# Kernel optimization log

Hardware: AMD Instinct MI355X
Metric: run time of the kernel (lower is better)

The kernel has to match this reference:

```python
import jax, jax.numpy as jnp
import numpy as np

VOCAB, F, H1, H2 = 64, 4096, 64, 32   # vocab size, featureVectorSize, hidden dims (hard-coded 64/32/1 in source)
NBBOX, NWORDS = 8192, 16


def _uniform(key, shape, fan_in):
    # torch nn.Linear default init: U(-1/sqrt(fan_in), 1/sqrt(fan_in))
    bound = 1.0 / np.sqrt(fan_in)
    return jax.random.uniform(key, shape, jnp.float32, -bound, bound)


def setup_inputs() -> dict:
    key = jax.random.key(0)
    ks = jax.random.split(key, 8)
    x = jax.random.normal(ks[0], (NBBOX, F), jnp.float32)
    words = jax.random.randint(ks[1], (NWORDS,), 0, VOCAB)  # indices of active word-models
    # Stacked per-word MLP params (one tiny MLP per vocab word)
    W1 = _uniform(ks[2], (VOCAB, F, H1), F)
    b1 = _uniform(ks[3], (VOCAB, H1), F)
    W2 = _uniform(ks[4], (VOCAB, H1, H2), H1)
    b2 = _uniform(ks[5], (VOCAB, H2), H1)
    W3 = _uniform(ks[6], (VOCAB, H2), H2)   # Linear(32,1) weight, squeezed to [VOCAB, H2]
    b3 = _uniform(ks[7], (VOCAB,), H2)
    return {"nBBox": NBBOX, "x": x, "words": words,
            "W1": W1, "b1": b1, "W2": W2, "b2": b2, "W3": W3, "b3": b3}


def reference(nBBox, x, words, W1, b1, W2, b2, W3, b3):
    # Gather the active word-models (dict lookup in the original)
    w1, c1 = W1[words], b1[words]          # [W,F,H1], [W,H1]
    w2, c2 = W2[words], b2[words]          # [W,H1,H2], [W,H2]
    w3, c3 = W3[words], b3[words]          # [W,H2], [W]
    # Batched 3-layer MLP over all active words at once (replaces Python loop)
    h1 = jax.nn.relu(jnp.einsum('bf,wfh->wbh', x, w1) + c1[:, None, :])   # [W,B,H1]
    h2 = jax.nn.relu(jnp.einsum('wbh,whk->wbk', h1, w2) + c2[:, None, :])  # [W,B,H2]
    logits = jnp.einsum('wbk,wk->wb', h2, w3) + c3[:, None]                # [W,B]
    # output = ones(nBBox,1) * prod_w sigmoid(logits_w)
    return jnp.prod(jax.nn.sigmoid(logits), axis=0)[:, None]               # [B,1]
```

## Files before the change

kernel.cpp:

```cpp
#include <hip/hip_runtime.h>
#include <stdint.h>
#include <math.h>

#define NBBOX 8192
#define FDIM  4096
#define H1DIM 64
#define H2DIM 32
#define NW    16

typedef __attribute__((ext_vector_type(8))) _Float16 f16x8;
typedef __attribute__((ext_vector_type(4))) float    f32x4;

typedef __attribute__((address_space(1))) void* gptr_t;
typedef __attribute__((address_space(3))) void* lptr_t;

__device__ __forceinline__ void g2l16(const void* g, void* l) {
    __builtin_amdgcn_global_load_lds((gptr_t)(uintptr_t)g,
                                     (lptr_t)(uint32_t)(uintptr_t)l,
                                     16, 0, 0);
}

__global__ __launch_bounds__(256) void prep(
    const float* __restrict__ x, _Float16* __restrict__ xh,
    const float* __restrict__ W1, const int* __restrict__ words,
    uint32_t* __restrict__ bth_u32)
{
    __shared__ uint32_t t[64 * 69];
    const int tid = threadIdx.x;

    if (blockIdx.x >= 512) {
        const int gid = (blockIdx.x - 512) * 256 + tid;
        const int idx = gid * 8;
        float4 a = *(const float4*)(x + idx);
        float4 b = *(const float4*)(x + idx + 4);
        f16x8 h;
        h[0] = (_Float16)a.x; h[1] = (_Float16)a.y; h[2] = (_Float16)a.z; h[3] = (_Float16)a.w;
        h[4] = (_Float16)b.x; h[5] = (_Float16)b.y; h[6] = (_Float16)b.z; h[7] = (_Float16)b.w;
        *(f16x8*)(xh + idx) = h;
        return;
    }

    const int wi = blockIdx.x >> 5;
    const int ft = blockIdx.x & 31;
    const int f0 = ft * 128;
    const int w  = words[wi];
    const int c    = tid & 63;
    const int fgrp = tid >> 6;

    const float* src = W1 + ((size_t)w * FDIM + f0) * H1DIM + c;
#pragma unroll
    for (int p = 0; p < 16; ++p) {
        const int f = fgrp * 2 + p * 8;
        float v0 = src[(size_t)f * H1DIM];
        float v1 = src[(size_t)(f + 1) * H1DIM];
        union { _Float16 h[2]; uint32_t u; } pk;
        pk.h[0] = (_Float16)v0; pk.h[1] = (_Float16)v1;
        t[c * 69 + (f >> 1)] = pk.u;
    }
    __syncthreads();
#pragma unroll
    for (int p = 0; p < 16; ++p) {
        const int cc = p * 4 + (tid >> 6);
        const int fd = tid & 63;
        bth_u32[(size_t)(wi * 64 + cc) * (FDIM / 2) + ft * 64 + fd] = t[cc * 69 + fd];
    }
}

__global__ __launch_bounds__(256, 2) void gemm_fused(
    const _Float16* __restrict__ xh, const _Float16* __restrict__ bth,
    const float* __restrict__ b1, const int* __restrict__ words,
    const float* __restrict__ W2, const float* __restrict__ b2,
    const float* __restrict__ W3, const float* __restrict__ b3,
    float* __restrict__ sig)
{
    __shared__ __align__(16) char smem[65536];
    float* tile = (float*)smem;

    const int mt   = blockIdx.x & 63;
    const int nt   = blockIdx.x >> 6;
    const int t    = threadIdx.x;
    const int w    = t >> 6;
    const int lane = t & 63;
    const int m0 = mt * 128, n0 = nt * 128;

    f32x4 acc[4][4] = {};

    const int lr = lane >> 3;
    const int cg = (lane & 7) ^ lr;
    const _Float16* Ag = xh  + (size_t)(m0 + w * 32 + lr) * FDIM + cg * 8;
    const _Float16* Bg = bth + (size_t)(n0 + w * 32 + lr) * FDIM + cg * 8;
    const int ldst = w * 32 * 128;

    const int wm = w >> 1, wn = w & 1;
    const int ml = lane & 15;
    const int qw = lane >> 4;

#pragma unroll
    for (int c = 0; c < 4; ++c) {
        g2l16(Ag + (size_t)(c * 8) * FDIM, smem + ldst + c * 1024);
        g2l16(Bg + (size_t)(c * 8) * FDIM, smem + 16384 + ldst + c * 1024);
    }
    __syncthreads();

    int cur = 0;
    for (int kt = 0; kt < 64; ++kt) {
        if (kt < 63) {
            const int nb = (cur ^ 1) * 32768;
            const size_t ko = (size_t)(kt + 1) * 64;
#pragma unroll
            for (int c = 0; c < 4; ++c) {
                g2l16(Ag + (size_t)(c * 8) * FDIM + ko, smem + nb + ldst + c * 1024);
                g2l16(Bg + (size_t)(c * 8) * FDIM + ko, smem + nb + 16384 + ldst + c * 1024);
            }
        }
        const _Float16* Ab = (const _Float16*)(smem + cur * 32768);
        const _Float16* Bb = (const _Float16*)(smem + cur * 32768 + 16384);
#pragma unroll
        for (int s = 0; s < 2; ++s) {
            f16x8 af[4], bfr[4];
#pragma unroll
            for (int i = 0; i < 4; ++i) {
                const int ra = wm * 64 + i * 16 + ml;
                af[i] = *(const f16x8*)&Ab[ra * 64 + (((s * 4 + qw) ^ (ml & 7)) * 8)];
            }
#pragma unroll
            for (int j = 0; j < 4; ++j) {
                const int rb = wn * 64 + j * 16 + ml;
                bfr[j] = *(const f16x8*)&Bb[rb * 64 + (((s * 4 + qw) ^ (ml & 7)) * 8)];
            }
#pragma unroll
            for (int i = 0; i < 4; ++i)
#pragma unroll
                for (int j = 0; j < 4; ++j)
                    acc[i][j] = __builtin_amdgcn_mfma_f32_16x16x32_f16(af[i], bfr[j], acc[i][j], 0, 0, 0);
        }
        __syncthreads();
        cur ^= 1;
    }

    const int q  = lane >> 4;
    const int wi = nt * 2 + wn;
    const int wv = __builtin_amdgcn_readfirstlane(words[wi]);
    float* tw = tile + w * 4096;

#pragma unroll
    for (int j = 0; j < 4; ++j) {
        const int col = j * 16 + ml;
        const float bias = b1[wv * H1DIM + col];
        const int c = col >> 2, e = col & 3;
#pragma unroll
        for (int i = 0; i < 4; ++i) {
#pragma unroll
            for (int r = 0; r < 4; ++r) {
                const int row = i * 16 + q * 4 + r;
                const int pos = ((c + row) & 7) | (c & 8);
                float v = acc[i][j][r] + bias;
                tw[row * 64 + pos * 4 + e] = v > 0.f ? v : 0.f;
            }
        }
    }

    const float* W2w = W2 + (size_t)wv * (H1DIM * H2DIM);
    float a2[H2DIM];
#pragma unroll
    for (int j = 0; j < H2DIM; ++j) a2[j] = 0.f;

#pragma unroll
    for (int c2 = 0; c2 < 16; ++c2) {
        const int pos = ((c2 + lane) & 7) | (c2 & 8);
        f32x4 h = *(const f32x4*)&tw[lane * 64 + pos * 4];
#pragma unroll
        for (int kk = 0; kk < 4; ++kk) {
            const float hv = h[kk];
            const int k = c2 * 4 + kk;
#pragma unroll
            for (int j = 0; j < H2DIM; ++j)
                a2[j] = fmaf(hv, W2w[k * H2DIM + j], a2[j]);
        }
    }

    float logit = b3[wv];
#pragma unroll
    for (int j = 0; j < H2DIM; ++j) {
        float h2 = a2[j] + b2[wv * H2DIM + j];
        h2 = h2 > 0.f ? h2 : 0.f;
        logit = fmaf(h2, W3[wv * H2DIM + j], logit);
    }
    sig[(size_t)wi * NBBOX + m0 + wm * 64 + lane] = 1.f / (1.f + expf(-logit));
}

__global__ void prod_k(const float* __restrict__ sig, float* __restrict__ out) {
    const int r = blockIdx.x * 256 + threadIdx.x;
    float p = 1.f;
#pragma unroll
    for (int wi = 0; wi < NW; ++wi) p *= sig[(size_t)wi * NBBOX + r];
    out[r] = p;
}

extern "C" void kernel_launch(void* const* d_in, const int* in_sizes, int n_in,
                              void* d_out, int out_size, void* d_ws, size_t ws_size,
                              hipStream_t stream)
{
    const float* x   = (const float*)d_in[1];
    const int* words = (const int*)  d_in[2];
    const float* W1  = (const float*)d_in[3];
    const float* b1  = (const float*)d_in[4];
    const float* W2  = (const float*)d_in[5];
    const float* b2  = (const float*)d_in[6];
    const float* W3  = (const float*)d_in[7];
    const float* b3  = (const float*)d_in[8];
    float* out = (float*)d_out;

    char* ws = (char*)d_ws;
    _Float16* xh  = (_Float16*)(ws);
    _Float16* bth = (_Float16*)(ws + 67108864);
    float*    sig = (float*)   (ws + 67108864 + 8388608);

    prep<<<512 + NBBOX * FDIM / 8 / 256, 256, 0, stream>>>(x, xh, W1, words, (uint32_t*)bth);
    gemm_fused<<<512, 256, 0, stream>>>(xh, bth, b1, words, W2, b2, W3, b3, sig);
    prod_k<<<NBBOX / 256, 256, 0, stream>>>(sig, out);
}
```

Baseline: 317.5 us.

## Fuse fp32-to-fp16 conversion of x into the GEMM load path

The separate pass that converted x to an fp16 workspace copy is removed. The GEMM now loads fp32 x tiles straight into registers during the prefetch, converts them to fp16, and writes them to swizzled LDS after the MFMA work for the current tile. This avoids writing and re-reading a 64MB fp16 copy. In exchange, each GEMM block reads x as fp32, which is twice the bytes, and that data is re-read by each of the 8 column tiles. The change also adds register pressure and swaps the async LDS loads for a register round trip.

Result: slower. 347.5 us (+9.4%).

```diff
diff --git a/kernel.cpp b/kernel.cpp
--- a/kernel.cpp
+++ b/kernel.cpp
@@ -20,26 +20,19 @@
                                      16, 0, 0);
 }
 
+__device__ __forceinline__ f16x8 cvt8(float4 a, float4 b) {
+    f16x8 h;
+    h[0] = (_Float16)a.x; h[1] = (_Float16)a.y; h[2] = (_Float16)a.z; h[3] = (_Float16)a.w;
+    h[4] = (_Float16)b.x; h[5] = (_Float16)b.y; h[6] = (_Float16)b.z; h[7] = (_Float16)b.w;
+    return h;
+}
+
 __global__ __launch_bounds__(256) void prep(
-    const float* __restrict__ x, _Float16* __restrict__ xh,
     const float* __restrict__ W1, const int* __restrict__ words,
     uint32_t* __restrict__ bth_u32)
 {
     __shared__ uint32_t t[64 * 69];
     const int tid = threadIdx.x;
-
-    if (blockIdx.x >= 512) {
-        const int gid = (blockIdx.x - 512) * 256 + tid;
-        const int idx = gid * 8;
-        float4 a = *(const float4*)(x + idx);
-        float4 b = *(const float4*)(x + idx + 4);
-        f16x8 h;
-        h[0] = (_Float16)a.x; h[1] = (_Float16)a.y; h[2] = (_Float16)a.z; h[3] = (_Float16)a.w;
-        h[4] = (_Float16)b.x; h[5] = (_Float16)b.y; h[6] = (_Float16)b.z; h[7] = (_Float16)b.w;
-        *(f16x8*)(xh + idx) = h;
-        return;
-    }
-
     const int wi = blockIdx.x >> 5;
     const int ft = blockIdx.x & 31;
     const int f0 = ft * 128;
@@ -67,7 +60,7 @@
 }
 
 __global__ __launch_bounds__(256, 2) void gemm_fused(
-    const _Float16* __restrict__ xh, const _Float16* __restrict__ bth,
+    const float* __restrict__ x, const _Float16* __restrict__ bth,
     const float* __restrict__ b1, const int* __restrict__ words,
     const float* __restrict__ W2, const float* __restrict__ b2,
     const float* __restrict__ W3, const float* __restrict__ b3,
@@ -86,31 +79,41 @@
     f32x4 acc[4][4] = {};
 
     const int lr = lane >> 3;
-    const int cg = (lane & 7) ^ lr;
-    const _Float16* Ag = xh  + (size_t)(m0 + w * 32 + lr) * FDIM + cg * 8;
-    const _Float16* Bg = bth + (size_t)(n0 + w * 32 + lr) * FDIM + cg * 8;
-    const int ldst = w * 32 * 128;
+    const int cg = lane & 7;
+    const float*    Ag = x   + (size_t)(m0 + w * 32 + lr) * FDIM + cg * 8;
+    const _Float16* Bg = bth + (size_t)(n0 + w * 32 + lr) * FDIM + ((cg ^ lr) * 8);
+    const int lwb = w * 4096;
 
     const int wm = w >> 1, wn = w & 1;
     const int ml = lane & 15;
     const int qw = lane >> 4;
 
-#pragma unroll
-    for (int c = 0; c < 4; ++c) {
-        g2l16(Ag + (size_t)(c * 8) * FDIM, smem + ldst + c * 1024);
-        g2l16(Bg + (size_t)(c * 8) * FDIM, smem + 16384 + ldst + c * 1024);
+    {
+        float4 a0[8];
+#pragma unroll
+        for (int c = 0; c < 4; ++c) {
+            a0[2 * c]     = *(const float4*)(Ag + (size_t)(c * 8) * FDIM);
+            a0[2 * c + 1] = *(const float4*)(Ag + (size_t)(c * 8) * FDIM + 4);
+            g2l16(Bg + (size_t)(c * 8) * FDIM, smem + 16384 + lwb + c * 1024);
+        }
+#pragma unroll
+        for (int c = 0; c < 4; ++c)
+            *(f16x8*)(smem + (w * 32 + c * 8 + lr) * 128 + ((cg ^ lr) * 16)) =
+                cvt8(a0[2 * c], a0[2 * c + 1]);
     }
     __syncthreads();
 
     int cur = 0;
     for (int kt = 0; kt < 64; ++kt) {
+        const int nb = (cur ^ 1) * 32768;
+        float4 ar[8];
         if (kt < 63) {
-            const int nb = (cur ^ 1) * 32768;
             const size_t ko = (size_t)(kt + 1) * 64;
 #pragma unroll
             for (int c = 0; c < 4; ++c) {
-                g2l16(Ag + (size_t)(c * 8) * FDIM + ko, smem + nb + ldst + c * 1024);
-                g2l16(Bg + (size_t)(c * 8) * FDIM + ko, smem + nb + 16384 + ldst + c * 1024);
+                ar[2 * c]     = *(const float4*)(Ag + (size_t)(c * 8) * FDIM + ko);
+                ar[2 * c + 1] = *(const float4*)(Ag + (size_t)(c * 8) * FDIM + ko + 4);
+                g2l16(Bg + (size_t)(c * 8) * FDIM + ko, smem + nb + 16384 + lwb + c * 1024);
             }
         }
         const _Float16* Ab = (const _Float16*)(smem + cur * 32768);
@@ -133,6 +136,12 @@
 #pragma unroll
                 for (int j = 0; j < 4; ++j)
                     acc[i][j] = __builtin_amdgcn_mfma_f32_16x16x32_f16(af[i], bfr[j], acc[i][j], 0, 0, 0);
+        }
+        if (kt < 63) {
+#pragma unroll
+            for (int c = 0; c < 4; ++c)
+                *(f16x8*)(smem + nb + (w * 32 + c * 8 + lr) * 128 + ((cg ^ lr) * 16)) =
+                    cvt8(ar[2 * c], ar[2 * c + 1]);
         }
         __syncthreads();
         cur ^= 1;
@@ -212,11 +221,10 @@
     float* out = (float*)d_out;
 
     char* ws = (char*)d_ws;
-    _Float16* xh  = (_Float16*)(ws);
-    _Float16* bth = (_Float16*)(ws + 67108864);
-    float*    sig = (float*)   (ws + 67108864 + 8388608);
-
-    prep<<<512 + NBBOX * FDIM / 8 / 256, 256, 0, stream>>>(x, xh, W1, words, (uint32_t*)bth);
-    gemm_fused<<<512, 256, 0, stream>>>(xh, bth, b1, words, W2, b2, W3, b3, sig);
+    _Float16* bth = (_Float16*)(ws);
+    float*    sig = (float*)   (ws + 8388608);
+
+    prep<<<512, 256, 0, stream>>>(W1, words, (uint32_t*)bth);
+    gemm_fused<<<512, 256, 0, stream>>>(x, bth, b1, words, W2, b2, W3, b3, sig);
     prod_k<<<NBBOX / 256, 256, 0, stream>>>(sig, out);
 }
```

## Merge prep, GEMM and product kernels into one persistent kernel with grid barriers

Applied to the files above, without the earlier changes.

Folds the three launches into a single 512-block kernel. Blocks first convert W1 and x to fp16, hit a software grid barrier built on an atomic counter, run the fused MLP GEMM, then hit a second barrier and compute the per-box product. This removes launch gaps and the tail of the large conversion grid. In exchange it relies on all 512 blocks being co-resident (2 per CU), adds spin-wait barrier cost and a memset launch, and makes the x conversion a grid-strided loop with fewer blocks.

New measurement: 482.7 us. 1.52x slower.

```diff
diff --git a/kernel.cpp b/kernel.cpp
--- a/kernel.cpp
+++ b/kernel.cpp
@@ -20,181 +20,198 @@
                                      16, 0, 0);
 }
 
-__global__ __launch_bounds__(256) void prep(
-    const float* __restrict__ x, _Float16* __restrict__ xh,
-    const float* __restrict__ W1, const int* __restrict__ words,
-    uint32_t* __restrict__ bth_u32)
-{
-    __shared__ uint32_t t[64 * 69];
-    const int tid = threadIdx.x;
-
-    if (blockIdx.x >= 512) {
-        const int gid = (blockIdx.x - 512) * 256 + tid;
-        const int idx = gid * 8;
-        float4 a = *(const float4*)(x + idx);
-        float4 b = *(const float4*)(x + idx + 4);
-        f16x8 h;
-        h[0] = (_Float16)a.x; h[1] = (_Float16)a.y; h[2] = (_Float16)a.z; h[3] = (_Float16)a.w;
-        h[4] = (_Float16)b.x; h[5] = (_Float16)b.y; h[6] = (_Float16)b.z; h[7] = (_Float16)b.w;
-        *(f16x8*)(xh + idx) = h;
-        return;
-    }
-
-    const int wi = blockIdx.x >> 5;
-    const int ft = blockIdx.x & 31;
-    const int f0 = ft * 128;
-    const int w  = words[wi];
-    const int c    = tid & 63;
-    const int fgrp = tid >> 6;
-
-    const float* src = W1 + ((size_t)w * FDIM + f0) * H1DIM + c;
-#pragma unroll
-    for (int p = 0; p < 16; ++p) {
-        const int f = fgrp * 2 + p * 8;
-        float v0 = src[(size_t)f * H1DIM];
-        float v1 = src[(size_t)(f + 1) * H1DIM];
-        union { _Float16 h[2]; uint32_t u; } pk;
-        pk.h[0] = (_Float16)v0; pk.h[1] = (_Float16)v1;
-        t[c * 69 + (f >> 1)] = pk.u;
-    }
+__device__ __forceinline__ void gbar(uint32_t* c) {
     __syncthreads();
-#pragma unroll
-    for (int p = 0; p < 16; ++p) {
-        const int cc = p * 4 + (tid >> 6);
-        const int fd = tid & 63;
-        bth_u32[(size_t)(wi * 64 + cc) * (FDIM / 2) + ft * 64 + fd] = t[cc * 69 + fd];
-    }
-}
-
-__global__ __launch_bounds__(256, 2) void gemm_fused(
-    const _Float16* __restrict__ xh, const _Float16* __restrict__ bth,
-    const float* __restrict__ b1, const int* __restrict__ words,
+    if (threadIdx.x == 0) {
+        __threadfence();
+        __hip_atomic_fetch_add(c, 1u, __ATOMIC_ACQ_REL, __HIP_MEMORY_SCOPE_AGENT);
+        while (__hip_atomic_load(c, __ATOMIC_ACQUIRE, __HIP_MEMORY_SCOPE_AGENT) < 512u)
+            __builtin_amdgcn_s_sleep(8);
+        __threadfence();
+    }
+    __syncthreads();
+}
+
+__global__ __launch_bounds__(256, 2) void mono(
+    const float* __restrict__ x, const int* __restrict__ words,
+    const float* __restrict__ W1, const float* __restrict__ b1,
     const float* __restrict__ W2, const float* __restrict__ b2,
     const float* __restrict__ W3, const float* __restrict__ b3,
-    float* __restrict__ sig)
+    _Float16* __restrict__ xh, uint32_t* __restrict__ bth_u32,
+    float* __restrict__ sig, uint32_t* __restrict__ bar,
+    float* __restrict__ out)
 {
     __shared__ __align__(16) char smem[65536];
-    float* tile = (float*)smem;
-
-    const int mt   = blockIdx.x & 63;
-    const int nt   = blockIdx.x >> 6;
-    const int t    = threadIdx.x;
-    const int w    = t >> 6;
-    const int lane = t & 63;
-    const int m0 = mt * 128, n0 = nt * 128;
-
-    f32x4 acc[4][4] = {};
-
-    const int lr = lane >> 3;
-    const int cg = (lane & 7) ^ lr;
-    const _Float16* Ag = xh  + (size_t)(m0 + w * 32 + lr) * FDIM + cg * 8;
-    const _Float16* Bg = bth + (size_t)(n0 + w * 32 + lr) * FDIM + cg * 8;
-    const int ldst = w * 32 * 128;
-
-    const int wm = w >> 1, wn = w & 1;
-    const int ml = lane & 15;
-    const int qw = lane >> 4;
-
-#pragma unroll
-    for (int c = 0; c < 4; ++c) {
-        g2l16(Ag + (size_t)(c * 8) * FDIM, smem + ldst + c * 1024);
-        g2l16(Bg + (size_t)(c * 8) * FDIM, smem + 16384 + ldst + c * 1024);
-    }
-    __syncthreads();
-
-    int cur = 0;
-    for (int kt = 0; kt < 64; ++kt) {
-        if (kt < 63) {
-            const int nb = (cur ^ 1) * 32768;
-            const size_t ko = (size_t)(kt + 1) * 64;
-#pragma unroll
-            for (int c = 0; c < 4; ++c) {
-                g2l16(Ag + (size_t)(c * 8) * FDIM + ko, smem + nb + ldst + c * 1024);
-                g2l16(Bg + (size_t)(c * 8) * FDIM + ko, smem + nb + 16384 + ldst + c * 1024);
-            }
-        }
-        const _Float16* Ab = (const _Float16*)(smem + cur * 32768);
-        const _Float16* Bb = (const _Float16*)(smem + cur * 32768 + 16384);
-#pragma unroll
-        for (int s = 0; s < 2; ++s) {
-            f16x8 af[4], bfr[4];
+    const int bx  = blockIdx.x;
+    const int tid = threadIdx.x;
+
+    {
+        uint32_t* t = (uint32_t*)smem;
+        const int wi = bx >> 5;
+        const int ft = bx & 31;
+        const int f0 = ft * 128;
+        const int wd = words[wi];
+        const int c    = tid & 63;
+        const int fgrp = tid >> 6;
+
+        const float* src = W1 + ((size_t)wd * FDIM + f0) * H1DIM + c;
+#pragma unroll
+        for (int p = 0; p < 16; ++p) {
+            const int f = fgrp * 2 + p * 8;
+            float v0 = src[(size_t)f * H1DIM];
+            float v1 = src[(size_t)(f + 1) * H1DIM];
+            union { _Float16 h[2]; uint32_t u; } pk;
+            pk.h[0] = (_Float16)v0; pk.h[1] = (_Float16)v1;
+            t[c * 69 + (f >> 1)] = pk.u;
+        }
+        __syncthreads();
+#pragma unroll
+        for (int p = 0; p < 16; ++p) {
+            const int cc = p * 4 + (tid >> 6);
+            const int fd = tid & 63;
+            bth_u32[(size_t)(wi * 64 + cc) * (FDIM / 2) + ft * 64 + fd] = t[cc * 69 + fd];
+        }
+    }
+    {
+        const int base = bx * 256 + tid;
+#pragma unroll 4
+        for (int it = 0; it < 32; ++it) {
+            const size_t idx = ((size_t)(base + it * 131072)) * 8;
+            float4 a = *(const float4*)(x + idx);
+            float4 b = *(const float4*)(x + idx + 4);
+            f16x8 h;
+            h[0] = (_Float16)a.x; h[1] = (_Float16)a.y; h[2] = (_Float16)a.z; h[3] = (_Float16)a.w;
+            h[4] = (_Float16)b.x; h[5] = (_Float16)b.y; h[6] = (_Float16)b.z; h[7] = (_Float16)b.w;
+            *(f16x8*)(xh + idx) = h;
+        }
+    }
+    gbar(bar);
+
+    {
+        const _Float16* bth = (const _Float16*)bth_u32;
+        float* tile = (float*)smem;
+
+        const int mt   = bx & 63;
+        const int nt   = bx >> 6;
+        const int w    = tid >> 6;
+        const int lane = tid & 63;
+        const int m0 = mt * 128, n0 = nt * 128;
+
+        f32x4 acc[4][4] = {};
+
+        const int lr = lane >> 3;
+        const int cg = (lane & 7) ^ lr;
+        const _Float16* Ag = xh  + (size_t)(m0 + w * 32 + lr) * FDIM + cg * 8;
+        const _Float16* Bg = bth + (size_t)(n0 + w * 32 + lr) * FDIM + cg * 8;
+        const int ldst = w * 32 * 128;
+
+        const int wm = w >> 1, wn = w & 1;
+        const int ml = lane & 15;
+        const int qw = lane >> 4;
+
+#pragma unroll
+        for (int c = 0; c < 4; ++c) {
+            g2l16(Ag + (size_t)(c * 8) * FDIM, smem + ldst + c * 1024);
+            g2l16(Bg + (size_t)(c * 8) * FDIM, smem + 16384 + ldst + c * 1024);
+        }
+        __syncthreads();
+
+        int cur = 0;
+        for (int kt = 0; kt < 64; ++kt) {
+            if (kt < 63) {
+                const int nb = (cur ^ 1) * 32768;
+                const size_t ko = (size_t)(kt + 1) * 64;
+#pragma unroll
+                for (int c = 0; c < 4; ++c) {
+                    g2l16(Ag + (size_t)(c * 8) * FDIM + ko, smem + nb + ldst + c * 1024);
+                    g2l16(Bg + (size_t)(c * 8) * FDIM + ko, smem + nb + 16384 + ldst + c * 1024);
+                }
+            }
+            const _Float16* Ab = (const _Float16*)(smem + cur * 32768);
+            const _Float16* Bb = (const _Float16*)(smem + cur * 32768 + 16384);
+#pragma unroll
+            for (int s = 0; s < 2; ++s) {
+                f16x8 af[4], bfr[4];
+#pragma unroll
+                for (int i = 0; i < 4; ++i) {
+                    const int ra = wm * 64 + i * 16 + ml;
+                    af[i] = *(const f16x8*)&Ab[ra * 64 + (((s * 4 + qw) ^ (ml & 7)) * 8)];
+                }
+#pragma unroll
+                for (int j = 0; j < 4; ++j) {
+                    const int rb = wn * 64 + j * 16 + ml;
+                    bfr[j] = *(const f16x8*)&Bb[rb * 64 + (((s * 4 + qw) ^ (ml & 7)) * 8)];
+                }
+#pragma unroll
+                for (int i = 0; i < 4; ++i)
+#pragma unroll
+                    for (int j = 0; j < 4; ++j)
+                        acc[i][j] = __builtin_amdgcn_mfma_f32_16x16x32_f16(af[i], bfr[j], acc[i][j], 0, 0, 0);
+            }
+            __syncthreads();
+            cur ^= 1;
+        }
+
+        const int q  = lane >> 4;
+        const int wi = nt * 2 + wn;
+        const int wv = __builtin_amdgcn_readfirstlane(words[wi]);
+        float* tw = tile + w * 4096;
+
+#pragma unroll
+        for (int j = 0; j < 4; ++j) {
+            const int col = j * 16 + ml;
+            const float bias = b1[wv * H1DIM + col];
+            const int c = col >> 2, e = col & 3;
 #pragma unroll
             for (int i = 0; i < 4; ++i) {
-                const int ra = wm * 64 + i * 16 + ml;
-                af[i] = *(const f16x8*)&Ab[ra * 64 + (((s * 4 + qw) ^ (ml & 7)) * 8)];
-            }
-#pragma unroll
-            for (int j = 0; j < 4; ++j) {
-                const int rb = wn * 64 + j * 16 + ml;
-                bfr[j] = *(const f16x8*)&Bb[rb * 64 + (((s * 4 + qw) ^ (ml & 7)) * 8)];
-            }
-#pragma unroll
-            for (int i = 0; i < 4; ++i)
-#pragma unroll
-                for (int j = 0; j < 4; ++j)
-                    acc[i][j] = __builtin_amdgcn_mfma_f32_16x16x32_f16(af[i], bfr[j], acc[i][j], 0, 0, 0);
-        }
-        __syncthreads();
-        cur ^= 1;
-    }
-
-    const int q  = lane >> 4;
-    const int wi = nt * 2 + wn;
-    const int wv = __builtin_amdgcn_readfirstlane(words[wi]);
-    float* tw = tile + w * 4096;
-
-#pragma unroll
-    for (int j = 0; j < 4; ++j) {
-        const int col = j * 16 + ml;
-        const float bias = b1[wv * H1DIM + col];
-        const int c = col >> 2, e = col & 3;
-#pragma unroll
-        for (int i = 0; i < 4; ++i) {
-#pragma unroll
-            for (int r = 0; r < 4; ++r) {
-                const int row = i * 16 + q * 4 + r;
-                const int pos = ((c + row) & 7) | (c & 8);
-                float v = acc[i][j][r] + bias;
-                tw[row * 64 + pos * 4 + e] = v > 0.f ? v : 0.f;
-            }
-        }
-    }
-
-    const float* W2w = W2 + (size_t)wv * (H1DIM * H2DIM);
-    float a2[H2DIM];
-#pragma unroll
-    for (int j = 0; j < H2DIM; ++j) a2[j] = 0.f;
-
-#pragma unroll
-    for (int c2 = 0; c2 < 16; ++c2) {
-        const int pos = ((c2 + lane) & 7) | (c2 & 8);
-        f32x4 h = *(const f32x4*)&tw[lane * 64 + pos * 4];
-#pragma unroll
-        for (int kk = 0; kk < 4; ++kk) {
-            const float hv = h[kk];
-            const int k = c2 * 4 + kk;
-#pragma unroll
-            for (int j = 0; j < H2DIM; ++j)
-                a2[j] = fmaf(hv, W2w[k * H2DIM + j], a2[j]);
-        }
-    }
-
-    float logit = b3[wv];
-#pragma unroll
-    for (int j = 0; j < H2DIM; ++j) {
-        float h2 = a2[j] + b2[wv * H2DIM + j];
-        h2 = h2 > 0.f ? h2 : 0.f;
-        logit = fmaf(h2, W3[wv * H2DIM + j], logit);
-    }
-    sig[(size_t)wi * NBBOX + m0 + wm * 64 + lane] = 1.f / (1.f + expf(-logit));
-}
-
-__global__ void prod_k(const float* __restrict__ sig, float* __restrict__ out) {
-    const int r = blockIdx.x * 256 + threadIdx.x;
-    float p = 1.f;
-#pragma unroll
-    for (int wi = 0; wi < NW; ++wi) p *= sig[(size_t)wi * NBBOX + r];
-    out[r] = p;
+#pragma unroll
+                for (int r = 0; r < 4; ++r) {
+                    const int row = i * 16 + q * 4 + r;
+                    const int pos = ((c + row) & 7) | (c & 8);
+                    float v = acc[i][j][r] + bias;
+                    tw[row * 64 + pos * 4 + e] = v > 0.f ? v : 0.f;
+                }
+            }
+        }
+
+        const float* W2w = W2 + (size_t)wv * (H1DIM * H2DIM);
+        float a2[H2DIM];
+#pragma unroll
+        for (int j = 0; j < H2DIM; ++j) a2[j] = 0.f;
+
+#pragma unroll
+        for (int c2 = 0; c2 < 16; ++c2) {
+            const int pos = ((c2 + lane) & 7) | (c2 & 8);
+            f32x4 h = *(const f32x4*)&tw[lane * 64 + pos * 4];
+#pragma unroll
+            for (int kk = 0; kk < 4; ++kk) {
+                const float hv = h[kk];
+                const int k = c2 * 4 + kk;
+#pragma unroll
+                for (int j = 0; j < H2DIM; ++j)
+                    a2[j] = fmaf(hv, W2w[k * H2DIM + j], a2[j]);
+            }
+        }
+
+        float logit = b3[wv];
+#pragma unroll
+        for (int j = 0; j < H2DIM; ++j) {
+            float h2 = a2[j] + b2[wv * H2DIM + j];
+            h2 = h2 > 0.f ? h2 : 0.f;
+            logit = fmaf(h2, W3[wv * H2DIM + j], logit);
+        }
+        sig[(size_t)wi * NBBOX + m0 + wm * 64 + lane] = 1.f / (1.f + expf(-logit));
+    }
+
+    gbar(bar + 1);
+
+    if (bx < NBBOX / 256) {
+        const int r = bx * 256 + tid;
+        float p = 1.f;
+#pragma unroll
+        for (int wi = 0; wi < NW; ++wi) p *= sig[(size_t)wi * NBBOX + r];
+        out[r] = p;
+    }
 }
 
 extern "C" void kernel_launch(void* const* d_in, const int* in_sizes, int n_in,
@@ -213,10 +230,11 @@
 
     char* ws = (char*)d_ws;
     _Float16* xh  = (_Float16*)(ws);
-    _Float16* bth = (_Float16*)(ws + 67108864);
+    uint32_t* bth = (uint32_t*)(ws + 67108864);
     float*    sig = (float*)   (ws + 67108864 + 8388608);
-
-    prep<<<512 + NBBOX * FDIM / 8 / 256, 256, 0, stream>>>(x, xh, W1, words, (uint32_t*)bth);
-    gemm_fused<<<512, 256, 0, stream>>>(xh, bth, b1, words, W2, b2, W3, b3, sig);
-    prod_k<<<NBBOX / 256, 256, 0, stream>>>(sig, out);
-}
+    uint32_t* bar = (uint32_t*)(ws + 67108864 + 8388608 + 524288);
+
+    hipMemsetAsync(bar, 0, 2 * sizeof(uint32_t), stream);
+    mono<<<512, 256, 0, stream>>>(x, words, W1, b1, W2, b2, W3, b3,
+                                  xh, bth, sig, bar, out);
+}
```
